# Kernel tuning notes

Measured on AMD Instinct MI355X. Metric: run time of the kernel, lower is better.

Reference implementation:

```python
import jax, jax.numpy as jnp
import numpy as np

D_MODEL = 512; DEPTH = 4; HEADS = 8; BUCKET = 256; N_HASHES = 4
INPUT_DIM = 32; SEQ = 2 * BUCKET; BATCH = 16; DH = D_MODEL // HEADS
N_BUCKETS = SEQ // BUCKET  # 2 (seq_len is forced to 2*bucket_size by pos_encoding)
SELF_ATTN_VALUE = -5e4  # TOKEN_SELF_ATTN_VALUE in reformer_pytorch


def layer_norm(x, g, b, eps=1e-5):
    m = jnp.mean(x, -1, keepdims=True)
    v = jnp.mean((x - m) ** 2, -1, keepdims=True)
    return (x - m) / jnp.sqrt(v + eps) * g + b


def look_one_back(x):
    # each chunk also attends to the previous chunk (circularly)
    prev = jnp.concatenate([x[:, -1:], x[:, :-1]], axis=1)
    return jnp.concatenate([x, prev], axis=2)


def lsh_attention(qk, v, rot):
    # qk, v: (B*H, T, DH); rot: (DH, N_HASHES, N_BUCKETS//2). Shared-QK LSH attention.
    B, T, d = qk.shape
    rotated = jnp.einsum('btf,fhi->bhti', qk, rot)                  # (B, nh, T, nb/2)
    rotated = jnp.concatenate([rotated, -rotated], axis=-1)        # (B, nh, T, nb)
    buckets = jnp.argmax(rotated, axis=-1)                          # (B, nh, T)
    offsets = (jnp.arange(N_HASHES) * N_BUCKETS)[None, :, None]
    buckets = (buckets + offsets).reshape(B, N_HASHES * T)
    ticker = jnp.arange(N_HASHES * T) % T
    bkt = T * buckets + ticker[None, :]                             # unique sort keys
    sticker = jnp.argsort(bkt, axis=-1)
    undo = jnp.argsort(sticker, axis=-1)
    st = sticker % T
    sqk = jnp.take_along_axis(qk, st[..., None], axis=1)            # (B, nh*T, d)
    sv = jnp.take_along_axis(v, st[..., None], axis=1)
    nch = N_HASHES * N_BUCKETS
    bq_t = st.reshape(B, nch, -1)
    bqk = sqk.reshape(B, nch, -1, d)
    bv = sv.reshape(B, nch, -1, d)
    bq = bqk
    bk = bqk / jnp.maximum(jnp.linalg.norm(bqk, axis=-1, keepdims=True), 1e-12)
    bk = look_one_back(bk)
    bv = look_one_back(bv)
    bkv_t = look_one_back(bq_t[..., None])[..., 0]
    dots = jnp.einsum('bcie,bcje->bcij', bq, bk) * (d ** -0.5)      # (B, nch, c, 2c)
    neg = -jnp.finfo(dots.dtype).max
    dots = jnp.where(bq_t[:, :, :, None] < bkv_t[:, :, None, :], neg, dots)   # causal
    dots = jnp.where(bq_t[:, :, :, None] == bkv_t[:, :, None, :], SELF_ATTN_VALUE, dots)  # de-prioritize self
    lse = jax.scipy.special.logsumexp(dots, axis=-1, keepdims=True)
    p = jnp.exp(dots - lse)
    bo = jnp.einsum('bcij,bcje->bcie', p, bv)
    so = bo.reshape(B, N_HASHES * T, d)
    sl = lse.reshape(B, N_HASHES * T)
    o = jnp.take_along_axis(so, undo[..., None], axis=1).reshape(B, N_HASHES, T, d)
    lg = jnp.take_along_axis(sl, undo, axis=1).reshape(B, N_HASHES, T, 1)
    w = jnp.exp(lg - jax.scipy.special.logsumexp(lg, axis=1, keepdims=True))  # combine hash rounds
    return jnp.sum(o * w, axis=1)


def lsh_self_attn(x, wqk, wv, wo, wo_b, rot):
    b, t, dm = x.shape
    split = lambda z: z.reshape(b, t, HEADS, DH).transpose(0, 2, 1, 3).reshape(b * HEADS, t, DH)
    o = lsh_attention(split(x @ wqk), split(x @ wv), rot)
    o = o.reshape(b, HEADS, t, DH).transpose(0, 2, 1, 3).reshape(b, t, dm)
    return o @ wo + wo_b


def setup_inputs() -> dict:
    key = jax.random.key(0)
    ks = jax.random.split(key, 12)
    f = lambda k, shape: jax.random.normal(k, shape, jnp.float32) * 0.02
    D, DEP, FF = D_MODEL, DEPTH, 4 * D_MODEL
    return {
        'x': jax.random.normal(ks[0], (BATCH, SEQ, INPUT_DIM), jnp.float32),
        'emb_w': f(ks[1], (INPUT_DIM, D)), 'emb_b': jnp.zeros((D,), jnp.float32),
        'pos': f(ks[2], (1, SEQ, D)),
        'ln1_g': jnp.ones((DEP, D), jnp.float32), 'ln1_b': jnp.zeros((DEP, D), jnp.float32),
        'wqk': f(ks[3], (DEP, D, D)), 'wv': f(ks[4], (DEP, D, D)),
        'wo': f(ks[5], (DEP, D, D)), 'wo_b': jnp.zeros((DEP, D), jnp.float32),
        'ln2_g': jnp.ones((DEP, D), jnp.float32), 'ln2_b': jnp.zeros((DEP, D), jnp.float32),
        'ff_w1': f(ks[6], (DEP, D, FF)), 'ff_b1': jnp.zeros((DEP, FF), jnp.float32),
        'ff_w2': f(ks[7], (DEP, FF, D)), 'ff_b2': jnp.zeros((DEP, D), jnp.float32),
        'rot': jax.random.normal(ks[8], (DEP, DH, N_HASHES, N_BUCKETS // 2), jnp.float32),
        'lnf_g': jnp.ones((D,), jnp.float32), 'lnf_b': jnp.zeros((D,), jnp.float32),
        'hw1': f(ks[9], (D, D // 2)), 'hb1': jnp.zeros((D // 2,), jnp.float32),
        'hln_g': jnp.ones((D // 2,), jnp.float32), 'hln_b': jnp.zeros((D // 2,), jnp.float32),
        'hw2': f(ks[10], (D // 2, 1)), 'hb2': jnp.zeros((1,), jnp.float32),
    }


def reference(x, emb_w, emb_b, pos, ln1_g, ln1_b, wqk, wv, wo, wo_b, ln2_g, ln2_b,
              ff_w1, ff_b1, ff_w2, ff_b2, rot, lnf_g, lnf_b, hw1, hb1, hln_g, hln_b, hw2, hb2):
    h = x @ emb_w + emb_b + pos
    # reversible residual stack (forward math): x1 += attn(norm(x2)); x2 += ff(norm(x1))
    x1 = h
    x2 = h
    for i in range(DEPTH):
        x1 = x1 + lsh_self_attn(layer_norm(x2, ln1_g[i], ln1_b[i]), wqk[i], wv[i], wo[i], wo_b[i], rot[i])
        hn = layer_norm(x1, ln2_g[i], ln2_b[i])
        x2 = x2 + jax.nn.gelu(hn @ ff_w1[i] + ff_b1[i], approximate=False) @ ff_w2[i] + ff_b2[i]
    h = 0.5 * (x1 + x2)
    h = layer_norm(h, lnf_g, lnf_b)[:, -1, :]
    h = jax.nn.relu(layer_norm(h @ hw1 + hb1, hln_g, hln_b))
    return h @ hw2 + hb2
```

## Files before the change

kernel.cpp:

```cpp
#include <hip/hip_runtime.h>
#include <hip/hip_fp16.h>
#include <cfloat>
#include <cstdint>

#define BB      16
#define TT      512
#define DD      512
#define HH      8
#define DHH     64
#define FFD     2048
#define BHH     128
#define NHASH   4
#define NCHUNK  8
#define CHUNKSZ 256
#define NLAYER  4

typedef unsigned short u16;
typedef unsigned int   u32;
typedef __attribute__((ext_vector_type(8))) short bfrag;
typedef __attribute__((ext_vector_type(4))) float f4x;
typedef __attribute__((ext_vector_type(16))) float f16x;

union FragU { u32 u[4]; uint4 v4; bfrag f; };

__device__ __forceinline__ unsigned pk_bf16(float a, float b) {
    union { float f; unsigned u; } x, y;
    x.f = a; y.f = b;
    unsigned lo = ((x.u + 0x7FFFu + ((x.u >> 16) & 1u)) >> 16) & 0xFFFFu;
    unsigned hi = (y.u + 0x7FFFu + ((y.u >> 16) & 1u)) & 0xFFFF0000u;
    return lo | hi;
}
__device__ __forceinline__ unsigned cvt_pk(float a, float b) {
    unsigned r;
    asm("v_cvt_pk_bf16_f32 %0, %1, %2" : "=v"(r) : "v"(a), "v"(b));
    return r;
}
__device__ __forceinline__ unsigned pkrtz(float a, float b) {
    unsigned r;
    asm("v_cvt_pkrtz_f16_f32 %0, %1, %2" : "=v"(r) : "v"(a), "v"(b));
    return r;
}
__device__ __forceinline__ u16 bf16_1(float a) {
    union { float f; unsigned u; } x; x.f = a;
    return (u16)((x.u + 0x7FFFu + ((x.u >> 16) & 1u)) >> 16);
}
__device__ __forceinline__ float b2f(u16 h) {
    union { unsigned u; float f; } x; x.u = ((unsigned)h) << 16; return x.f;
}

__device__ __forceinline__ void gload16(const u16* g, u16* l) {
    __builtin_amdgcn_global_load_lds(
        (const __attribute__((address_space(1))) u32*)g,
        (__attribute__((address_space(3))) u32*)l, 16, 0, 0);
}

__global__ __launch_bounds__(256)
void embed_kernel(const float* __restrict__ x, const float* __restrict__ ew,
                  const float* __restrict__ eb, const float* __restrict__ pos,
                  float* __restrict__ x1, float* __restrict__ x2)
{
    const int row = blockIdx.x;
    const int t = row & (TT - 1);
    __shared__ float xr[32];
    if (threadIdx.x < 32) xr[threadIdx.x] = x[row * 32 + threadIdx.x];
    __syncthreads();
    for (int d = threadIdx.x; d < DD; d += 256) {
        float s = eb[d] + pos[t * DD + d];
        #pragma unroll
        for (int k = 0; k < 32; ++k) s = fmaf(xr[k], ew[k * DD + d], s);
        x1[(size_t)row * DD + d] = s;
        x2[(size_t)row * DD + d] = s;
    }
}

__global__ __launch_bounds__(256)
void ln_kernel(const float* __restrict__ in, const float* __restrict__ g,
               const float* __restrict__ bta, float* __restrict__ out,
               u16* __restrict__ outh)
{
    const int row = blockIdx.x * 4 + (threadIdx.x >> 6);
    const int lane = threadIdx.x & 63;
    const float* r = in + (size_t)row * DD;
    float vals[8];
    float s = 0.0f;
    #pragma unroll
    for (int i = 0; i < 8; ++i) { vals[i] = r[i * 64 + lane]; s += vals[i]; }
    #pragma unroll
    for (int o = 1; o < 64; o <<= 1) s += __shfl_xor(s, o);
    const float mean = s * (1.0f / 512.0f);
    float vs = 0.0f;
    #pragma unroll
    for (int i = 0; i < 8; ++i) { float d = vals[i] - mean; vs += d * d; }
    #pragma unroll
    for (int o = 1; o < 64; o <<= 1) vs += __shfl_xor(vs, o);
    const float rstd = rsqrtf(vs * (1.0f / 512.0f) + 1e-5f);
    float* orow = out + (size_t)row * DD;
    u16* hrow = outh + (size_t)row * DD;
    #pragma unroll
    for (int i = 0; i < 8; ++i) {
        const int d = i * 64 + lane;
        const float y = (vals[i] - mean) * rstd * g[d] + bta[d];
        orow[d] = y;
        hrow[d] = bf16_1(y);
    }
}

__global__ __launch_bounds__(256)
void prep_weights(const float* __restrict__ wqk, const float* __restrict__ wv,
                  const float* __restrict__ wo, const float* __restrict__ ffw1,
                  const float* __restrict__ ffw2,
                  u16* __restrict__ wqkT, u16* __restrict__ wvT,
                  u16* __restrict__ woT, u16* __restrict__ w1T,
                  u16* __restrict__ w2T)
{
    const int id = blockIdx.x;
    const float* in; u16* outp; int K, N, kt, nt;
    if (id < 3072) {
        const int fam = id >> 10;
        const int r = id & 1023;
        const int L = r >> 8, t = r & 255;
        K = 512; N = 512;
        const size_t off = (size_t)L * 512 * 512;
        in   = (fam == 0 ? wqk  : fam == 1 ? wv  : wo ) + off;
        outp = (fam == 0 ? wqkT : fam == 1 ? wvT : woT) + off;
        kt = (t & 15) << 5; nt = (t >> 4) << 5;
    } else if (id < 7168) {
        const int r = id - 3072;
        const int L = r >> 10, t = r & 1023;
        K = 512; N = 2048;
        in = ffw1 + (size_t)L * 512 * 2048;
        outp = w1T + (size_t)L * 2048 * 512;
        kt = (t & 15) << 5; nt = (t >> 4) << 5;
    } else {
        const int r = id - 7168;
        const int L = r >> 10, t = r & 1023;
        K = 2048; N = 512;
        in = ffw2 + (size_t)L * 2048 * 512;
        outp = w2T + (size_t)L * 512 * 2048;
        kt = (t & 63) << 5; nt = (t >> 6) << 5;
    }
    __shared__ float tile[32][33];
    const int rr = threadIdx.x >> 3, c4 = (threadIdx.x & 7) * 4;
    const float4 v4 = *(const float4*)(in + (size_t)(kt + rr) * N + nt + c4);
    tile[rr][c4 + 0] = v4.x; tile[rr][c4 + 1] = v4.y;
    tile[rr][c4 + 2] = v4.z; tile[rr][c4 + 3] = v4.w;
    __syncthreads();
    uint2 p;
    p.x = pk_bf16(tile[c4 + 0][rr], tile[c4 + 1][rr]);
    p.y = pk_bf16(tile[c4 + 2][rr], tile[c4 + 3][rr]);
    *(uint2*)(outp + (size_t)(nt + rr) * K + kt + c4) = p;
}

__global__ __launch_bounds__(256)
void wrot_kernel(const float* __restrict__ wqk, const float* __restrict__ rot,
                 float* __restrict__ wrotAll)
{
    const int hh = blockIdx.x, L = blockIdx.y;
    const int head = hh >> 2, h = hh & 3;
    __shared__ float rc[64];
    if (threadIdx.x < 64)
        rc[threadIdx.x] = rot[((size_t)L * 64 + threadIdx.x) * 4 + h];
    __syncthreads();
    for (int f = threadIdx.x; f < 512; f += 256) {
        const float* wrow = wqk + (size_t)L * 512 * 512 + (size_t)f * 512 + head * 64;
        float s = 0.0f;
        #pragma unroll
        for (int d = 0; d < 64; d += 4) {
            const float4 w4 = *(const float4*)(wrow + d);
            s += w4.x * rc[d] + w4.y * rc[d + 1] + w4.z * rc[d + 2] + w4.w * rc[d + 3];
        }
        wrotAll[((size_t)L * 512 + f) * 32 + hh] = s;
    }
}

__global__ __launch_bounds__(256)
void rot_gemm(const float* __restrict__ A, const float* __restrict__ Wr,
              float* __restrict__ C)
{
    __shared__ float As[64][36];
    __shared__ float Ws[32][36];
    const int m0 = blockIdx.x * 64;
    const int r = threadIdx.x >> 2, cg = threadIdx.x & 3;
    float acc[8] = {};
    for (int f0 = 0; f0 < 512; f0 += 32) {
        __syncthreads();
        {
            const int lr = threadIdx.x >> 2, lc = (threadIdx.x & 3) * 8;
            const float* ap = A + (size_t)(m0 + lr) * 512 + f0 + lc;
            *(float4*)&As[lr][lc]     = ((const float4*)ap)[0];
            *(float4*)&As[lr][lc + 4] = ((const float4*)ap)[1];
            const int wr = threadIdx.x >> 3, wc = (threadIdx.x & 7) * 4;
            *(float4*)&Ws[wr][wc] = *(const float4*)(Wr + (size_t)(f0 + wr) * 32 + wc);
        }
        __syncthreads();
        #pragma unroll
        for (int kk = 0; kk < 32; ++kk) {
            const float a = As[r][kk];
            #pragma unroll
            for (int c = 0; c < 8; ++c)
                acc[c] = fmaf(a, Ws[kk][cg * 8 + c], acc[c]);
        }
    }
    float* crow = C + (size_t)(m0 + r) * 32 + cg * 8;
    *(float4*)crow       = make_float4(acc[0], acc[1], acc[2], acc[3]);
    *(float4*)(crow + 4) = make_float4(acc[4], acc[5], acc[6], acc[7]);
}

__device__ __forceinline__ float gelu1(float v) {
    return 0.5f * v * (1.0f + erff(v * 0.70710678118654752440f));
}
__device__ __forceinline__ int swz_row(int r, int BK) {
    return (BK == 32) ? ((r & 3) ^ ((r >> 2) & 3)) : (r & 7);
}

template<int BM, int BN, int BK, bool GELU, bool ADD, bool BIAS, bool OUTBF, bool QKL>
__global__ __launch_bounds__(256)
void gemm_bf16(const u16* __restrict__ A, const u16* __restrict__ WT,
               const float* __restrict__ bias, const float* __restrict__ addsrc,
               float* __restrict__ Cf, u16* __restrict__ Cb,
               int M, int N, int K)
{
    constexpr int NCH = BK / 8;
    constexpr int CPA = BM * NCH / 256;
    constexpr int CPB = BN * NCH / 256;
    constexpr int MR = BM / 32, NR = BN / 32, KR = BK / 32;
    __shared__ __align__(16) u16 Abuf[2][BM * BK];
    __shared__ __align__(16) u16 Bbuf[2][BN * BK];
    const int tid = threadIdx.x;
    const int m0 = blockIdx.x * BM, n0 = blockIdx.y * BN;

    const u16* aSrc[CPA]; const u16* bSrc[CPB];
    #pragma unroll
    for (int i = 0; i < CPA; ++i) {
        const int s = tid + i * 256, row = s / NCH, ch = s % NCH;
        aSrc[i] = A + (size_t)(m0 + row) * K + (ch ^ swz_row(row, BK)) * 8;
    }
    #pragma unroll
    for (int i = 0; i < CPB; ++i) {
        const int s = tid + i * 256, row = s / NCH, ch = s % NCH;
        bSrc[i] = WT + (size_t)(n0 + row) * K + (ch ^ swz_row(row, BK)) * 8;
    }

    auto STAGE = [&](int bufi, int koff) {
        #pragma unroll
        for (int i = 0; i < CPA; ++i)
            gload16(aSrc[i] + koff, &Abuf[bufi][(tid + i * 256) * 8]);
        #pragma unroll
        for (int i = 0; i < CPB; ++i)
            gload16(bSrc[i] + koff, &Bbuf[bufi][(tid + i * 256) * 8]);
    };

    const int l = tid & 63, wv_ = tid >> 6;
    const int wm = (wv_ >> 1) * (BM / 2);
    const int wn = (wv_ & 1) * (BN / 2);
    const int fr = l & 15, fc = l >> 4;

    f4x acc[MR][NR] = {};
    const int nK = K / BK;
    STAGE(0, 0);
    for (int ks = 0; ks < nK; ++ks) {
        __syncthreads();
        if (ks + 1 < nK) STAGE((ks + 1) & 1, (ks + 1) * BK);
        const u16* Ab = Abuf[ks & 1];
        const u16* Bb = Bbuf[ks & 1];
        FragU af[MR][KR], bf_[NR][KR];
        #pragma unroll
        for (int i = 0; i < MR; ++i)
            #pragma unroll
            for (int u = 0; u < KR; ++u) {
                const int r = wm + i * 16 + fr;
                af[i][u].v4 = *(const uint4*)((const char*)Ab +
                    (size_t)r * (2 * BK) + (((u * 4 + fc) ^ swz_row(r, BK)) << 4));
            }
        #pragma unroll
        for (int j = 0; j < NR; ++j)
            #pragma unroll
            for (int u = 0; u < KR; ++u) {
                const int r = wn + j * 16 + fr;
                bf_[j][u].v4 = *(const uint4*)((const char*)Bb +
                    (size_t)r * (2 * BK) + (((u * 4 + fc) ^ swz_row(r, BK)) << 4));
            }
        #pragma unroll
        for (int u = 0; u < KR; ++u)
            #pragma unroll
            for (int i = 0; i < MR; ++i)
                #pragma unroll
                for (int j = 0; j < NR; ++j)
                    acc[i][j] = __builtin_amdgcn_mfma_f32_16x16x32_bf16(
                        af[i][u].f, bf_[j][u].f, acc[i][j], 0, 0, 0);
    }

    #pragma unroll
    for (int i = 0; i < MR; ++i) {
        #pragma unroll
        for (int q = 0; q < 4; ++q) {
            const int row = m0 + wm + i * 16 + fc * 4 + q;
            #pragma unroll
            for (int j = 0; j < NR; ++j) {
                const int col = n0 + wn + j * 16 + fr;
                float vx = acc[i][j][q];
                if constexpr (BIAS) vx += bias[col];
                if constexpr (GELU) vx = gelu1(vx);
                if constexpr (ADD) vx += addsrc[(size_t)row * N + col];
                if constexpr (QKL) {
                    const int bq = row >> 9, tq = row & 511;
                    const int hq = col >> 6, dq = col & 63;
                    Cb[(((size_t)(bq * 8 + hq) * 512) + tq) * 64 + dq] = bf16_1(vx);
                } else if constexpr (OUTBF) {
                    Cb[(size_t)row * N + col] = bf16_1(vx);
                } else {
                    Cf[(size_t)row * N + col] = vx;
                }
            }
        }
    }
}

__global__ __launch_bounds__(256)
void knorm_kernel(const u16* __restrict__ qkh, u16* __restrict__ qkn,
                  float* __restrict__ qnrm)
{
    const int g = blockIdx.x * 16 + (threadIdx.x >> 4);
    const int li = threadIdx.x & 15;
    const uint2 raw = *(const uint2*)(qkh + (size_t)g * 64 + li * 4);
    const float v0 = b2f((u16)(raw.x & 0xffff)), v1 = b2f((u16)(raw.x >> 16));
    const float v2 = b2f((u16)(raw.y & 0xffff)), v3 = b2f((u16)(raw.y >> 16));
    float ss = v0 * v0 + v1 * v1 + v2 * v2 + v3 * v3;
    ss += __shfl_xor(ss, 1); ss += __shfl_xor(ss, 2);
    ss += __shfl_xor(ss, 4); ss += __shfl_xor(ss, 8);
    const float qn = sqrtf(ss);
    const float rv = 1.0f / fmaxf(qn, 1e-12f);
    uint2 o;
    o.x = cvt_pk(v0 * rv, v1 * rv);
    o.y = cvt_pk(v2 * rv, v3 * rv);
    *(uint2*)(qkn + (size_t)g * 64 + li * 4) = o;
    if (li == 0) qnrm[g] = qn;
}

__global__ __launch_bounds__(512)
void bucket_sort_kernel(const float* __restrict__ rotated, int* __restrict__ st)
{
    const int h = blockIdx.x, bh = blockIdx.y;
    const int b = bh >> 3, head = bh & 7;
    const int t = threadIdx.x;
    __shared__ int zcnt[8];
    const float r = rotated[((size_t)(b * TT + t)) * 32 + head * 4 + h];
    const int bit = (r < 0.0f) ? 1 : 0;
    const int wid = t >> 6, lane = t & 63;
    const unsigned long long zm = __ballot(bit == 0);
    if (lane == 0) zcnt[wid] = __popcll(zm);
    __syncthreads();
    int zoff = 0, Z = 0;
    #pragma unroll
    for (int w = 0; w < 8; ++w) { const int cn = zcnt[w]; if (w < wid) zoff += cn; Z += cn; }
    const int zpre = __popcll(zm & ((1ull << lane) - 1ull));
    const int dst = (bit == 0) ? (zoff + zpre)
                               : (Z + (wid * 64 - zoff) + (lane - zpre));
    st[((size_t)bh * NHASH + h) * TT + dst] = t;
}

__global__ __launch_bounds__(256)
void lsh_attn_mfma(const u16* __restrict__ qkn, const u16* __restrict__ v,
                   const float* __restrict__ qnrm, const int* __restrict__ st,
                   __half* __restrict__ o_hash, float* __restrict__ lse_hash)
{
    const int cc = blockIdx.x, bh = blockIdx.y;
    const int b = bh >> 3, head = bh & 7;
    const int h = cc >> 1, c = cc & 1;
    const int pcc = (cc + 7) & 7;
    const int hp = pcc >> 1, cp = pcc & 1;
    const int tid = threadIdx.x;
    const int w = tid >> 6;
    const int lane = tid & 63;
    const int l31 = lane & 31;
    const int hi = lane >> 5;
    const int* stb = st + (size_t)bh * (NHASH * TT);
    const size_t vbase = ((size_t)b * TT) * DD + head * DHH;
    const u16* qknb = qkn + (size_t)bh * TT * DHH;

    __shared__ __align__(16) u16 Kbf[64 * 64];
    __shared__ __align__(16) u16 VTbf[64 * 64];
    __shared__ __align__(16) int ktl[64];
    __shared__ float lW[4][64];
    __shared__ int qtW[4][64];
    __shared__ float Ost[4][32 * 33];

    int q_t[2]; float aC[2], mnat[2];
    uint4 QF4[2][4];
    #pragma unroll
    for (int qt = 0; qt < 2; ++qt) {
        const int qtk = stb[h * TT + c * CHUNKSZ + w * 64 + qt * 32 + l31];
        q_t[qt] = qtk;
        const float qn = qnrm[(size_t)bh * TT + qtk];
        mnat[qt] = qn * 0.125f;
        aC[qt]   = qn * 0.1803368801111137f;
        const u16* qrow = qknb + (size_t)qtk * DHH;
        #pragma unroll
        for (int ds = 0; ds < 4; ++ds)
            QF4[qt][ds] = *(const uint4*)(qrow + ds * 16 + hi * 8);
    }

    f16x acc[2][2] = {};
    float lacc[2] = {0.f, 0.f};
    const int k8 = tid >> 2;
    const int q4 = tid & 3;

    auto gather = [&](int t8, uint4& kv0, uint4& kv1, uint4& vv0, uint4& vv1,
                      int& ktc) {
        const int kj = t8 * 64 + k8;
        const int k_t = (kj < CHUNKSZ) ? stb[h * TT + c * CHUNKSZ + kj]
                                       : stb[hp * TT + cp * CHUNKSZ + (kj - CHUNKSZ)];
        ktc = k_t;
        const u16* krow = qknb + (size_t)k_t * DHH + q4 * 16;
        const u16* vrow = v + vbase + (size_t)k_t * DD + q4 * 16;
        kv0 = ((const uint4*)krow)[0]; kv1 = ((const uint4*)krow)[1];
        vv0 = ((const uint4*)vrow)[0]; vv1 = ((const uint4*)vrow)[1];
    };

    uint4 kv0, kv1, vv0, vv1; int ktc;
    gather(0, kv0, kv1, vv0, vv1, ktc);

    for (int kt8 = 0; kt8 < 8; ++kt8) {
        __syncthreads();
        {
            const int rbase = k8 * 128 + q4 * 32;
            const int swz = (k8 & 7) << 4;
            *(uint4*)((char*)Kbf + ((rbase)      ^ swz)) = kv0;
            *(uint4*)((char*)Kbf + ((rbase + 16) ^ swz)) = kv1;
        }
        {
            const unsigned vu[8] = {vv0.x, vv0.y, vv0.z, vv0.w,
                                    vv1.x, vv1.y, vv1.z, vv1.w};
            #pragma unroll
            for (int i = 0; i < 16; ++i) {
                const int d = q4 * 16 + i;
                const u16 hv = (u16)((i & 1) ? (vu[i >> 1] >> 16) : (vu[i >> 1] & 0xffff));
                *(u16*)((char*)VTbf + ((d * 128 + k8 * 2) ^ ((d & 7) << 4))) = hv;
            }
        }
        if (q4 == 0) ktl[k8] = ktc;
        __syncthreads();

        const int t8n = (kt8 < 7) ? kt8 + 1 : 0;
        gather(t8n, kv0, kv1, vv0, vv1, ktc);

        #pragma unroll
        for (int kt = 0; kt < 2; ++kt) {
            int4 kt4[4];
            #pragma unroll
            for (int j = 0; j < 4; ++j)
                kt4[j] = *(const int4*)&ktl[kt * 32 + 8 * j + 4 * hi];
            const int* ktvp = (const int*)kt4;
            FragU KA[4];
            #pragma unroll
            for (int ds = 0; ds < 4; ++ds) {
                const int row = kt * 32 + l31;
                KA[ds].v4 = *(const uint4*)((const char*)Kbf +
                    ((row * 128 + ds * 32 + hi * 16) ^ ((row & 7) << 4)));
            }
            FragU VA[2][2];
            #pragma unroll
            for (int dt = 0; dt < 2; ++dt)
                #pragma unroll
                for (int u = 0; u < 2; ++u) {
                    const int row = dt * 32 + l31;
                    const int ks = kt * 2 + u;
                    VA[dt][u].v4 = *(const uint4*)((const char*)VTbf +
                        ((row * 128 + ks * 32 + hi * 16) ^ ((row & 7) << 4)));
                }
            #pragma unroll
            for (int qt = 0; qt < 2; ++qt) {
                f16x s = {0.f,0.f,0.f,0.f,0.f,0.f,0.f,0.f,
                          0.f,0.f,0.f,0.f,0.f,0.f,0.f,0.f};
                #pragma unroll
                for (int ds = 0; ds < 4; ++ds) {
                    FragU qf; qf.v4 = QF4[qt][ds];
                    s = __builtin_amdgcn_mfma_f32_32x32x16_bf16(KA[ds].f, qf.f, s, 0, 0, 0);
                }
                const float a = aC[qt];
                float pv[16];
                #pragma unroll
                for (int i = 0; i < 16; ++i) {
                    const float e = exp2f(fmaf(s[i], a, -a));
                    const float p = (q_t[qt] > ktvp[i]) ? e : 0.0f;
                    pv[i] = p;
                    lacc[qt] += p;
                }
                unsigned P2[8];
                #pragma unroll
                for (int g = 0; g < 4; ++g) {
                    P2[2*g]   = cvt_pk(pv[4*g],   pv[4*g+1]);
                    P2[2*g+1] = cvt_pk(pv[4*g+2], pv[4*g+3]);
                }
                #pragma unroll
                for (int u = 0; u < 2; ++u) {
                    unsigned a0 = P2[4*u + 0], b0 = P2[4*u + 2];
                    unsigned a1 = P2[4*u + 1], b1 = P2[4*u + 3];
                    asm("v_permlane32_swap_b32 %0, %1" : "+v"(a0), "+v"(b0));
                    asm("v_permlane32_swap_b32 %0, %1" : "+v"(a1), "+v"(b1));
                    FragU bfv;
                    bfv.u[0] = a0; bfv.u[1] = a1; bfv.u[2] = b0; bfv.u[3] = b1;
                    #pragma unroll
                    for (int dt = 0; dt < 2; ++dt)
                        acc[dt][qt] = __builtin_amdgcn_mfma_f32_32x32x16_bf16(
                            VA[dt][u].f, bfv.f, acc[dt][qt], 0, 0, 0);
                }
            }
        }
    }

    float invl[2];
    #pragma unroll
    for (int qt = 0; qt < 2; ++qt) {
        const float lt = lacc[qt] + __shfl_xor(lacc[qt], 32);
        invl[qt] = (lt > 0.f) ? 1.0f / lt : 0.0f;
        const float lse = (lt > 0.f) ? (mnat[qt] + logf(lt)) : -5.0e4f;
        if (hi == 0) {
            lW[w][qt * 32 + l31] = lt;
            qtW[w][qt * 32 + l31] = q_t[qt];
            lse_hash[(size_t)(bh * NHASH + h) * TT + q_t[qt]] = lse;
        }
    }
    __syncthreads();

    float* ost = Ost[w];
    #pragma unroll
    for (int qt = 0; qt < 2; ++qt)
        #pragma unroll
        for (int dt = 0; dt < 2; ++dt) {
            #pragma unroll
            for (int r = 0; r < 16; ++r) {
                const int row = (r & 3) + 8 * (r >> 2) + 4 * hi;
                ost[row * 33 + l31] = acc[dt][qt][r] * invl[qt];
            }
            const int qq = lane >> 1, h2 = lane & 1;
            const int qglob = qtW[w][qt * 32 + qq];
            const float lq = lW[w][qt * 32 + qq];
            float ov[16];
            #pragma unroll
            for (int i = 0; i < 16; ++i)
                ov[i] = ost[(h2 * 16 + i) * 33 + qq];
            __half* orow = o_hash + ((size_t)(bh * NHASH + h) * TT + qglob) * DHH
                         + dt * 32 + h2 * 16;
            if (lq > 0.f) {
                uint4 o0, o1;
                o0.x = pkrtz(ov[0],  ov[1]);  o0.y = pkrtz(ov[2],  ov[3]);
                o0.z = pkrtz(ov[4],  ov[5]);  o0.w = pkrtz(ov[6],  ov[7]);
                o1.x = pkrtz(ov[8],  ov[9]);  o1.y = pkrtz(ov[10], ov[11]);
                o1.z = pkrtz(ov[12], ov[13]); o1.w = pkrtz(ov[14], ov[15]);
                ((uint4*)orow)[0] = o0;
                ((uint4*)orow)[1] = o1;
            } else {
                const u16* vr = v + vbase + (size_t)qglob * DD + dt * 32 + h2 * 16;
                uint4 o0, o1;
                o0.x = pkrtz(b2f(vr[0]),  b2f(vr[1]));
                o0.y = pkrtz(b2f(vr[2]),  b2f(vr[3]));
                o0.z = pkrtz(b2f(vr[4]),  b2f(vr[5]));
                o0.w = pkrtz(b2f(vr[6]),  b2f(vr[7]));
                o1.x = pkrtz(b2f(vr[8]),  b2f(vr[9]));
                o1.y = pkrtz(b2f(vr[10]), b2f(vr[11]));
                o1.z = pkrtz(b2f(vr[12]), b2f(vr[13]));
                o1.w = pkrtz(b2f(vr[14]), b2f(vr[15]));
                ((uint4*)orow)[0] = o0;
                ((uint4*)orow)[1] = o1;
            }
        }
}

__global__ __launch_bounds__(256)
void combine_kernel(const __half* __restrict__ o_hash, const float* __restrict__ lse_hash,
                    u16* __restrict__ am)
{
    const int idx = blockIdx.x * 4 + (threadIdx.x >> 6);
    const int lane = threadIdx.x & 63;
    const int bh = idx >> 9, t = idx & 511;
    const int b = bh >> 3, head = bh & 7;
    const float ls0 = lse_hash[(size_t)(bh * NHASH + 0) * TT + t];
    const float ls1 = lse_hash[(size_t)(bh * NHASH + 1) * TT + t];
    const float ls2 = lse_hash[(size_t)(bh * NHASH + 2) * TT + t];
    const float ls3 = lse_hash[(size_t)(bh * NHASH + 3) * TT + t];
    const float M = fmaxf(fmaxf(ls0, ls1), fmaxf(ls2, ls3));
    const float e0 = __expf(ls0 - M), e1 = __expf(ls1 - M);
    const float e2 = __expf(ls2 - M), e3 = __expf(ls3 - M);
    const float inv = 1.0f / (e0 + e1 + e2 + e3);
    const float o =
        (e0 * __half2float(o_hash[((size_t)((bh * NHASH + 0) * TT + t)) * DHH + lane]) +
         e1 * __half2float(o_hash[((size_t)((bh * NHASH + 1) * TT + t)) * DHH + lane]) +
         e2 * __half2float(o_hash[((size_t)((bh * NHASH + 2) * TT + t)) * DHH + lane]) +
         e3 * __half2float(o_hash[((size_t)((bh * NHASH + 3) * TT + t)) * DHH + lane])) * inv;
    am[((size_t)(b * TT + t)) * DD + head * DHH + lane] = bf16_1(o);
}

__device__ __forceinline__ float block_sum256(float v, volatile float* red)
{
    const int lane = threadIdx.x & 63, wid = threadIdx.x >> 6;
    #pragma unroll
    for (int o = 1; o < 64; o <<= 1) v += __shfl_xor(v, o);
    __syncthreads();
    if (lane == 0) red[wid] = v;
    __syncthreads();
    return red[0] + red[1] + red[2] + red[3];
}

__global__ __launch_bounds__(256)
void head_kernel(const float* __restrict__ x1, const float* __restrict__ x2,
                 const float* __restrict__ lnfg, const float* __restrict__ lnfb,
                 const float* __restrict__ hw1, const float* __restrict__ hb1,
                 const float* __restrict__ hlng, const float* __restrict__ hlnb,
                 const float* __restrict__ hw2, const float* __restrict__ hb2,
                 float* __restrict__ out)
{
    __shared__ float nrow[512];
    __shared__ float red[4];
    const int b = blockIdx.x, tid = threadIdx.x;
    const size_t roff = ((size_t)b * TT + (TT - 1)) * DD;
    const float v0 = 0.5f * (x1[roff + tid] + x2[roff + tid]);
    const float v1 = 0.5f * (x1[roff + 256 + tid] + x2[roff + 256 + tid]);
    const float mean = block_sum256(v0 + v1, red) * (1.0f / 512.0f);
    const float d0 = v0 - mean, d1 = v1 - mean;
    const float var = block_sum256(d0 * d0 + d1 * d1, red) * (1.0f / 512.0f);
    const float rstd = rsqrtf(var + 1e-5f);
    nrow[tid]       = d0 * rstd * lnfg[tid] + lnfb[tid];
    nrow[tid + 256] = d1 * rstd * lnfg[tid + 256] + lnfb[tid + 256];
    __syncthreads();
    float a = hb1[tid];
    for (int k = 0; k < 512; ++k) a = fmaf(nrow[k], hw1[(size_t)k * 256 + tid], a);
    const float m2 = block_sum256(a, red) * (1.0f / 256.0f);
    const float dd = a - m2;
    const float var2 = block_sum256(dd * dd, red) * (1.0f / 256.0f);
    float y = dd * rsqrtf(var2 + 1e-5f) * hlng[tid] + hlnb[tid];
    y = fmaxf(y, 0.0f);
    const float osum = block_sum256(y * hw2[tid], red);
    if (tid == 0) out[b] = osum + hb2[0];
}

extern "C" void kernel_launch(void* const* d_in, const int* in_sizes, int n_in,
                              void* d_out, int out_size, void* d_ws, size_t ws_size,
                              hipStream_t stream)
{
    (void)in_sizes; (void)n_in; (void)out_size; (void)ws_size;
    const float* x    = (const float*)d_in[0];
    const float* embw = (const float*)d_in[1];
    const float* embb = (const float*)d_in[2];
    const float* pos  = (const float*)d_in[3];
    const float* ln1g = (const float*)d_in[4];
    const float* ln1b = (const float*)d_in[5];
    const float* wqk  = (const float*)d_in[6];
    const float* wv   = (const float*)d_in[7];
    const float* wo   = (const float*)d_in[8];
    const float* wob  = (const float*)d_in[9];
    const float* ln2g = (const float*)d_in[10];
    const float* ln2b = (const float*)d_in[11];
    const float* ffw1 = (const float*)d_in[12];
    const float* ffb1 = (const float*)d_in[13];
    const float* ffw2 = (const float*)d_in[14];
    const float* ffb2 = (const float*)d_in[15];
    const float* rot  = (const float*)d_in[16];
    const float* lnfg = (const float*)d_in[17];
    const float* lnfb = (const float*)d_in[18];
    const float* hw1  = (const float*)d_in[19];
    const float* hb1  = (const float*)d_in[20];
    const float* hlng = (const float*)d_in[21];
    const float* hlnb = (const float*)d_in[22];
    const float* hw2  = (const float*)d_in[23];
    const float* hb2  = (const float*)d_in[24];
    float* out = (float*)d_out;

    const size_t SZ_BTD = (size_t)BB * TT * DD;
    const size_t SZ_OH  = (size_t)BHH * NHASH * TT * DHH;

    char* p = (char*)d_ws;
    float* x1b = (float*)p;  p += SZ_BTD * 4;
    float* x2b = (float*)p;  p += SZ_BTD * 4;
    float* xnb = (float*)p;  p += SZ_BTD * 4;
    u16*   vbh = (u16*)p;    p += SZ_BTD * 2;
    u16*   xnbh = (u16*)p;   p += SZ_BTD * 2;
    u16*   qkh  = (u16*)p;   p += SZ_BTD * 2;
    u16*   qknb = (u16*)p;   p += (size_t)BHH * TT * DHH * 2;
    float* qnrm = (float*)p; p += (size_t)BHH * TT * 4;
    float* rotated = (float*)p; p += (size_t)BB * TT * 32 * 4;
    __half* ohash = (__half*)p;
    u16*    ffmid = (u16*)p;
    p += SZ_OH * 2;
    float* lseb  = (float*)p; p += (size_t)BHH * NHASH * TT * 4;
    int*   stb   = (int*)p;   p += (size_t)BHH * NHASH * TT * 4;
    u16* wqkT = (u16*)p; p += (size_t)NLAYER * DD * DD * 2;
    u16* wvT  = (u16*)p; p += (size_t)NLAYER * DD * DD * 2;
    u16* woT  = (u16*)p; p += (size_t)NLAYER * DD * DD * 2;
    u16* w1T  = (u16*)p; p += (size_t)NLAYER * DD * FFD * 2;
    u16* w2T  = (u16*)p; p += (size_t)NLAYER * FFD * DD * 2;
    float* wrotAll = (float*)p; p += (size_t)NLAYER * DD * 32 * 4;
    u16* amb = (u16*)xnb;

    prep_weights<<<11264, 256, 0, stream>>>(wqk, wv, wo, ffw1, ffw2,
                                            wqkT, wvT, woT, w1T, w2T);
    wrot_kernel<<<dim3(32, NLAYER), 256, 0, stream>>>(wqk, rot, wrotAll);

    embed_kernel<<<BB * TT, 256, 0, stream>>>(x, embw, embb, pos, x1b, x2b);

    for (int L = 0; L < NLAYER; ++L) {
        const size_t w512 = (size_t)L * DD * DD;
        const size_t wff  = (size_t)L * DD * FFD;

        ln_kernel<<<2048, 256, 0, stream>>>(x2b, ln1g + L * DD, ln1b + L * DD, xnb, xnbh);
        rot_gemm<<<128, 256, 0, stream>>>(xnb, wrotAll + (size_t)L * DD * 32, rotated);
        gemm_bf16<64, 64, 64, false, false, false, true, true><<<dim3(128, 8), 256, 0, stream>>>(
            xnbh, wqkT + w512, nullptr, nullptr, nullptr, qkh, BB * TT, DD, DD);
        gemm_bf16<64, 64, 64, false, false, false, true, false><<<dim3(128, 8), 256, 0, stream>>>(
            xnbh, wvT + w512, nullptr, nullptr, nullptr, vbh, BB * TT, DD, DD);
        bucket_sort_kernel<<<dim3(NHASH, BHH), 512, 0, stream>>>(rotated, stb);
        knorm_kernel<<<4096, 256, 0, stream>>>(qkh, qknb, qnrm);
        lsh_attn_mfma<<<dim3(NCHUNK, BHH), 256, 0, stream>>>(
            qknb, vbh, qnrm, stb, ohash, lseb);
        combine_kernel<<<16384, 256, 0, stream>>>(ohash, lseb, amb);
        gemm_bf16<64, 64, 64, false, true, true, false, false><<<dim3(128, 8), 256, 0, stream>>>(
            amb, woT + w512, wob + L * DD, x1b, x1b, nullptr, BB * TT, DD, DD);

        ln_kernel<<<2048, 256, 0, stream>>>(x1b, ln2g + L * DD, ln2b + L * DD, xnb, xnbh);
        gemm_bf16<128, 128, 32, true, false, true, true, false><<<dim3(64, 16), 256, 0, stream>>>(
            xnbh, w1T + wff, ffb1 + L * FFD, nullptr, nullptr, ffmid, BB * TT, FFD, DD);
        gemm_bf16<64, 64, 64, false, true, true, false, false><<<dim3(128, 8), 256, 0, stream>>>(
            ffmid, w2T + wff, ffb2 + L * DD, x2b, x2b, nullptr, BB * TT, DD, FFD);
    }

    head_kernel<<<16, 256, 0, stream>>>(x1b, x2b, lnfg, lnfb, hw1, hb1,
                                        hlng, hlnb, hw2, hb2, out);
}
```

Baseline: 1.032 ms.

## Use 512-thread LSH attention blocks with one query tile per wave

The LSH attention kernel now runs 512 threads per block. Each wave handles a single 32-query tile instead of two, which halves per-wave accumulator registers, and the K/V gather is split across twice as many threads. The output epilogue now uses permlane swaps to write rows directly, dropping the shared-memory transpose staging and its extra barrier. Separately, the second layer norm skips its unused fp32 output store. The larger block gives more waves per CU but makes each block's barriers wait on more waves.

Measured after the change: 947.9 us. 1.09x faster.

```diff
diff --git a/kernel.cpp b/kernel.cpp
--- a/kernel.cpp
+++ b/kernel.cpp
@@ -94,13 +94,12 @@
     #pragma unroll
     for (int o = 1; o < 64; o <<= 1) vs += __shfl_xor(vs, o);
     const float rstd = rsqrtf(vs * (1.0f / 512.0f) + 1e-5f);
-    float* orow = out + (size_t)row * DD;
     u16* hrow = outh + (size_t)row * DD;
     #pragma unroll
     for (int i = 0; i < 8; ++i) {
         const int d = i * 64 + lane;
         const float y = (vals[i] - mean) * rstd * g[d] + bta[d];
-        orow[d] = y;
+        if (out != nullptr) out[(size_t)row * DD + d] = y;
         hrow[d] = bf16_1(y);
     }
 }
@@ -359,7 +358,7 @@
     st[((size_t)bh * NHASH + h) * TT + dst] = t;
 }
 
-__global__ __launch_bounds__(256)
+__global__ __launch_bounds__(512, 4)
 void lsh_attn_mfma(const u16* __restrict__ qkn, const u16* __restrict__ v,
                    const float* __restrict__ qnrm, const int* __restrict__ st,
                    __half* __restrict__ o_hash, float* __restrict__ lse_hash)
@@ -381,68 +380,53 @@
     __shared__ __align__(16) u16 Kbf[64 * 64];
     __shared__ __align__(16) u16 VTbf[64 * 64];
     __shared__ __align__(16) int ktl[64];
-    __shared__ float lW[4][64];
-    __shared__ int qtW[4][64];
-    __shared__ float Ost[4][32 * 33];
-
-    int q_t[2]; float aC[2], mnat[2];
-    uint4 QF4[2][4];
-    #pragma unroll
-    for (int qt = 0; qt < 2; ++qt) {
-        const int qtk = stb[h * TT + c * CHUNKSZ + w * 64 + qt * 32 + l31];
-        q_t[qt] = qtk;
-        const float qn = qnrm[(size_t)bh * TT + qtk];
-        mnat[qt] = qn * 0.125f;
-        aC[qt]   = qn * 0.1803368801111137f;
-        const u16* qrow = qknb + (size_t)qtk * DHH;
+
+    const int q_t = stb[h * TT + c * CHUNKSZ + w * 32 + l31];
+    const float qn = qnrm[(size_t)bh * TT + q_t];
+    const float mnat = qn * 0.125f;
+    const float aC = qn * 0.1803368801111137f;
+    uint4 QF4[4];
+    {
+        const u16* qrow = qknb + (size_t)q_t * DHH;
         #pragma unroll
         for (int ds = 0; ds < 4; ++ds)
-            QF4[qt][ds] = *(const uint4*)(qrow + ds * 16 + hi * 8);
-    }
-
-    f16x acc[2][2] = {};
-    float lacc[2] = {0.f, 0.f};
-    const int k8 = tid >> 2;
-    const int q4 = tid & 3;
-
-    auto gather = [&](int t8, uint4& kv0, uint4& kv1, uint4& vv0, uint4& vv1,
-                      int& ktc) {
+            QF4[ds] = *(const uint4*)(qrow + ds * 16 + hi * 8);
+    }
+
+    f16x acc[2] = {};
+    float lacc = 0.f;
+    const int k8 = tid >> 3;
+    const int c8 = tid & 7;
+
+    auto gather = [&](int t8, uint4& kc, uint4& vc, int& ktc) {
         const int kj = t8 * 64 + k8;
         const int k_t = (kj < CHUNKSZ) ? stb[h * TT + c * CHUNKSZ + kj]
                                        : stb[hp * TT + cp * CHUNKSZ + (kj - CHUNKSZ)];
         ktc = k_t;
-        const u16* krow = qknb + (size_t)k_t * DHH + q4 * 16;
-        const u16* vrow = v + vbase + (size_t)k_t * DD + q4 * 16;
-        kv0 = ((const uint4*)krow)[0]; kv1 = ((const uint4*)krow)[1];
-        vv0 = ((const uint4*)vrow)[0]; vv1 = ((const uint4*)vrow)[1];
+        kc = *(const uint4*)(qknb + (size_t)k_t * DHH + c8 * 8);
+        vc = *(const uint4*)(v + vbase + (size_t)k_t * DD + c8 * 8);
     };
 
-    uint4 kv0, kv1, vv0, vv1; int ktc;
-    gather(0, kv0, kv1, vv0, vv1, ktc);
+    uint4 kc, vc; int ktc;
+    gather(0, kc, vc, ktc);
 
     for (int kt8 = 0; kt8 < 8; ++kt8) {
         __syncthreads();
+        *(uint4*)((char*)Kbf + ((k8 * 128 + c8 * 16) ^ ((k8 & 7) << 4))) = kc;
         {
-            const int rbase = k8 * 128 + q4 * 32;
-            const int swz = (k8 & 7) << 4;
-            *(uint4*)((char*)Kbf + ((rbase)      ^ swz)) = kv0;
-            *(uint4*)((char*)Kbf + ((rbase + 16) ^ swz)) = kv1;
-        }
-        {
-            const unsigned vu[8] = {vv0.x, vv0.y, vv0.z, vv0.w,
-                                    vv1.x, vv1.y, vv1.z, vv1.w};
-            #pragma unroll
-            for (int i = 0; i < 16; ++i) {
-                const int d = q4 * 16 + i;
+            const unsigned vu[4] = {vc.x, vc.y, vc.z, vc.w};
+            #pragma unroll
+            for (int i = 0; i < 8; ++i) {
+                const int d = c8 * 8 + i;
                 const u16 hv = (u16)((i & 1) ? (vu[i >> 1] >> 16) : (vu[i >> 1] & 0xffff));
-                *(u16*)((char*)VTbf + ((d * 128 + k8 * 2) ^ ((d & 7) << 4))) = hv;
-            }
-        }
-        if (q4 == 0) ktl[k8] = ktc;
+                *(u16*)((char*)VTbf + ((d * 128 + k8 * 2) ^ (i << 4))) = hv;
+            }
+        }
+        if (c8 == 0) ktl[k8] = ktc;
         __syncthreads();
 
         const int t8n = (kt8 < 7) ? kt8 + 1 : 0;
-        gather(t8n, kv0, kv1, vv0, vv1, ktc);
+        gather(t8n, kc, vc, ktc);
 
         #pragma unroll
         for (int kt = 0; kt < 2; ++kt) {
@@ -468,103 +452,79 @@
                     VA[dt][u].v4 = *(const uint4*)((const char*)VTbf +
                         ((row * 128 + ks * 32 + hi * 16) ^ ((row & 7) << 4)));
                 }
-            #pragma unroll
-            for (int qt = 0; qt < 2; ++qt) {
-                f16x s = {0.f,0.f,0.f,0.f,0.f,0.f,0.f,0.f,
-                          0.f,0.f,0.f,0.f,0.f,0.f,0.f,0.f};
+            f16x s = {0.f,0.f,0.f,0.f,0.f,0.f,0.f,0.f,
+                      0.f,0.f,0.f,0.f,0.f,0.f,0.f,0.f};
+            #pragma unroll
+            for (int ds = 0; ds < 4; ++ds) {
+                FragU qf; qf.v4 = QF4[ds];
+                s = __builtin_amdgcn_mfma_f32_32x32x16_bf16(KA[ds].f, qf.f, s, 0, 0, 0);
+            }
+            float pv[16];
+            #pragma unroll
+            for (int i = 0; i < 16; ++i) {
+                const float e = exp2f(fmaf(s[i], aC, -aC));
+                const float p = (q_t > ktvp[i]) ? e : 0.0f;
+                pv[i] = p;
+                lacc += p;
+            }
+            unsigned P2[8];
+            #pragma unroll
+            for (int g = 0; g < 4; ++g) {
+                P2[2*g]   = cvt_pk(pv[4*g],   pv[4*g+1]);
+                P2[2*g+1] = cvt_pk(pv[4*g+2], pv[4*g+3]);
+            }
+            #pragma unroll
+            for (int u = 0; u < 2; ++u) {
+                unsigned a0 = P2[4*u + 0], b0 = P2[4*u + 2];
+                unsigned a1 = P2[4*u + 1], b1 = P2[4*u + 3];
+                asm("v_permlane32_swap_b32 %0, %1" : "+v"(a0), "+v"(b0));
+                asm("v_permlane32_swap_b32 %0, %1" : "+v"(a1), "+v"(b1));
+                FragU bfv;
+                bfv.u[0] = a0; bfv.u[1] = a1; bfv.u[2] = b0; bfv.u[3] = b1;
                 #pragma unroll
-                for (int ds = 0; ds < 4; ++ds) {
-                    FragU qf; qf.v4 = QF4[qt][ds];
-                    s = __builtin_amdgcn_mfma_f32_32x32x16_bf16(KA[ds].f, qf.f, s, 0, 0, 0);
-                }
-                const float a = aC[qt];
-                float pv[16];
-                #pragma unroll
-                for (int i = 0; i < 16; ++i) {
-                    const float e = exp2f(fmaf(s[i], a, -a));
-                    const float p = (q_t[qt] > ktvp[i]) ? e : 0.0f;
-                    pv[i] = p;
-                    lacc[qt] += p;
-                }
-                unsigned P2[8];
-                #pragma unroll
-                for (int g = 0; g < 4; ++g) {
-                    P2[2*g]   = cvt_pk(pv[4*g],   pv[4*g+1]);
-                    P2[2*g+1] = cvt_pk(pv[4*g+2], pv[4*g+3]);
-                }
-                #pragma unroll
-                for (int u = 0; u < 2; ++u) {
-                    unsigned a0 = P2[4*u + 0], b0 = P2[4*u + 2];
-                    unsigned a1 = P2[4*u + 1], b1 = P2[4*u + 3];
-                    asm("v_permlane32_swap_b32 %0, %1" : "+v"(a0), "+v"(b0));
-                    asm("v_permlane32_swap_b32 %0, %1" : "+v"(a1), "+v"(b1));
-                    FragU bfv;
-                    bfv.u[0] = a0; bfv.u[1] = a1; bfv.u[2] = b0; bfv.u[3] = b1;
-                    #pragma unroll
-                    for (int dt = 0; dt < 2; ++dt)
-                        acc[dt][qt] = __builtin_amdgcn_mfma_f32_32x32x16_bf16(
-                            VA[dt][u].f, bfv.f, acc[dt][qt], 0, 0, 0);
-                }
-            }
-        }
-    }
-
-    float invl[2];
-    #pragma unroll
-    for (int qt = 0; qt < 2; ++qt) {
-        const float lt = lacc[qt] + __shfl_xor(lacc[qt], 32);
-        invl[qt] = (lt > 0.f) ? 1.0f / lt : 0.0f;
-        const float lse = (lt > 0.f) ? (mnat[qt] + logf(lt)) : -5.0e4f;
-        if (hi == 0) {
-            lW[w][qt * 32 + l31] = lt;
-            qtW[w][qt * 32 + l31] = q_t[qt];
-            lse_hash[(size_t)(bh * NHASH + h) * TT + q_t[qt]] = lse;
-        }
-    }
-    __syncthreads();
-
-    float* ost = Ost[w];
-    #pragma unroll
-    for (int qt = 0; qt < 2; ++qt)
-        #pragma unroll
-        for (int dt = 0; dt < 2; ++dt) {
-            #pragma unroll
-            for (int r = 0; r < 16; ++r) {
-                const int row = (r & 3) + 8 * (r >> 2) + 4 * hi;
-                ost[row * 33 + l31] = acc[dt][qt][r] * invl[qt];
-            }
-            const int qq = lane >> 1, h2 = lane & 1;
-            const int qglob = qtW[w][qt * 32 + qq];
-            const float lq = lW[w][qt * 32 + qq];
-            float ov[16];
-            #pragma unroll
-            for (int i = 0; i < 16; ++i)
-                ov[i] = ost[(h2 * 16 + i) * 33 + qq];
-            __half* orow = o_hash + ((size_t)(bh * NHASH + h) * TT + qglob) * DHH
-                         + dt * 32 + h2 * 16;
-            if (lq > 0.f) {
-                uint4 o0, o1;
-                o0.x = pkrtz(ov[0],  ov[1]);  o0.y = pkrtz(ov[2],  ov[3]);
-                o0.z = pkrtz(ov[4],  ov[5]);  o0.w = pkrtz(ov[6],  ov[7]);
-                o1.x = pkrtz(ov[8],  ov[9]);  o1.y = pkrtz(ov[10], ov[11]);
-                o1.z = pkrtz(ov[12], ov[13]); o1.w = pkrtz(ov[14], ov[15]);
-                ((uint4*)orow)[0] = o0;
-                ((uint4*)orow)[1] = o1;
-            } else {
-                const u16* vr = v + vbase + (size_t)qglob * DD + dt * 32 + h2 * 16;
-                uint4 o0, o1;
-                o0.x = pkrtz(b2f(vr[0]),  b2f(vr[1]));
-                o0.y = pkrtz(b2f(vr[2]),  b2f(vr[3]));
-                o0.z = pkrtz(b2f(vr[4]),  b2f(vr[5]));
-                o0.w = pkrtz(b2f(vr[6]),  b2f(vr[7]));
-                o1.x = pkrtz(b2f(vr[8]),  b2f(vr[9]));
-                o1.y = pkrtz(b2f(vr[10]), b2f(vr[11]));
-                o1.z = pkrtz(b2f(vr[12]), b2f(vr[13]));
-                o1.w = pkrtz(b2f(vr[14]), b2f(vr[15]));
-                ((uint4*)orow)[0] = o0;
-                ((uint4*)orow)[1] = o1;
-            }
-        }
+                for (int dt = 0; dt < 2; ++dt)
+                    acc[dt] = __builtin_amdgcn_mfma_f32_32x32x16_bf16(
+                        VA[dt][u].f, bfv.f, acc[dt], 0, 0, 0);
+            }
+        }
+    }
+
+    const float lt = lacc + __shfl_xor(lacc, 32);
+    const float invl = (lt > 0.f) ? 1.0f / lt : 0.0f;
+    if (hi == 0) {
+        const float lse = (lt > 0.f) ? (mnat + logf(lt)) : -5.0e4f;
+        lse_hash[(size_t)(bh * NHASH + h) * TT + q_t] = lse;
+    }
+    unsigned wa[8], wb[8];
+    #pragma unroll
+    for (int m = 0; m < 8; ++m) {
+        wa[m] = pkrtz(acc[0][2*m] * invl, acc[0][2*m+1] * invl);
+        wb[m] = pkrtz(acc[1][2*m] * invl, acc[1][2*m+1] * invl);
+    }
+    #pragma unroll
+    for (int m = 0; m < 8; ++m)
+        asm("v_permlane32_swap_b32 %0, %1" : "+v"(wa[m]), "+v"(wb[m]));
+    __half* orow = o_hash + ((size_t)(bh * NHASH + h) * TT + q_t) * DHH + hi * 32;
+    if (lt > 0.f) {
+        #pragma unroll
+        for (int g = 0; g < 4; ++g) {
+            uint4 o;
+            o.x = wa[2*g]; o.y = wa[2*g+1];
+            o.z = wb[2*g]; o.w = wb[2*g+1];
+            ((uint4*)orow)[g] = o;
+        }
+    } else {
+        const u16* vr = v + vbase + (size_t)q_t * DD + hi * 32;
+        #pragma unroll
+        for (int g = 0; g < 4; ++g) {
+            uint4 o;
+            o.x = pkrtz(b2f(vr[8*g+0]), b2f(vr[8*g+1]));
+            o.y = pkrtz(b2f(vr[8*g+2]), b2f(vr[8*g+3]));
+            o.z = pkrtz(b2f(vr[8*g+4]), b2f(vr[8*g+5]));
+            o.w = pkrtz(b2f(vr[8*g+6]), b2f(vr[8*g+7]));
+            ((uint4*)orow)[g] = o;
+        }
+    }
 }
 
 __global__ __launch_bounds__(256)
@@ -710,13 +670,13 @@
             xnbh, wvT + w512, nullptr, nullptr, nullptr, vbh, BB * TT, DD, DD);
         bucket_sort_kernel<<<dim3(NHASH, BHH), 512, 0, stream>>>(rotated, stb);
         knorm_kernel<<<4096, 256, 0, stream>>>(qkh, qknb, qnrm);
-        lsh_attn_mfma<<<dim3(NCHUNK, BHH), 256, 0, stream>>>(
+        lsh_attn_mfma<<<dim3(NCHUNK, BHH), 512, 0, stream>>>(
             qknb, vbh, qnrm, stb, ohash, lseb);
         combine_kernel<<<16384, 256, 0, stream>>>(ohash, lseb, amb);
         gemm_bf16<64, 64, 64, false, true, true, false, false><<<dim3(128, 8), 256, 0, stream>>>(
             amb, woT + w512, wob + L * DD, x1b, x1b, nullptr, BB * TT, DD, DD);
 
-        ln_kernel<<<2048, 256, 0, stream>>>(x1b, ln2g + L * DD, ln2b + L * DD, xnb, xnbh);
+        ln_kernel<<<2048, 256, 0, stream>>>(x1b, ln2g + L * DD, ln2b + L * DD, nullptr, xnbh);
         gemm_bf16<128, 128, 32, true, false, true, true, false><<<dim3(64, 16), 256, 0, stream>>>(
             xnbh, w1T + wff, ffb1 + L * FFD, nullptr, nullptr, ffmid, BB * TT, FFD, DD);
         gemm_bf16<64, 64, 64, false, true, true, false, false><<<dim3(128, 8), 256, 0, stream>>>(
```
